# Kernel tuning notes

Measured on AMD Instinct MI355X. Metric: run time of the kernel, lower is better.

The kernel has to match this reference:

```python
import jax, jax.numpy as jnp
import numpy as np

B, D, M, C = 8192, 2048, 8, 1000

def setup_inputs() -> dict:
    key = jax.random.key(0)
    k1, k2, k3, k4, k5 = jax.random.split(key, 5)
    scale = 1.0 / np.sqrt(D)
    return {
        "x": jax.random.normal(k1, (B, D), dtype=jnp.float32),
        "model_weights": jax.random.normal(k2, (M, D, C), dtype=jnp.float32) * scale,
        "model_bias": jax.random.normal(k3, (M, C), dtype=jnp.float32) * 0.01,
        "resnet_weight": jax.random.normal(k4, (D, M * C), dtype=jnp.float32) * scale,
        "resnet_bias": jax.random.normal(k5, (M * C,), dtype=jnp.float32) * 0.01,
    }

def reference(x, model_weights, model_bias, resnet_weight, resnet_bias):
    # Per-submodel logits: [B, M, C]
    outputs = jnp.einsum("bd,mdc->bmc", x, model_weights) + model_bias[None, :, :]
    # Fusion weights from the weighting network: [B, M, C]
    w = (x @ resnet_weight + resnet_bias).reshape(x.shape[0], model_weights.shape[0], model_weights.shape[2])
    # Fused weighted sum over models (replaces the triple Python loop): [B, C]
    result = jnp.sum(outputs * w, axis=1)
    return result
```

## Files before the change

### kernel.cpp

```cpp
#include <hip/hip_runtime.h>
#include <hip/hip_bf16.h>
#include <stdint.h>

#define BDIM 8192
#define DDIM 2048
#define MDIM 8
#define CDIM 1000
#define CPAD 1024
#define NPAD 8192

typedef __attribute__((ext_vector_type(8))) short bf16x8;
typedef __attribute__((ext_vector_type(4))) float f32x4;

__device__ __forceinline__ unsigned short f2bf(float f) {
    union { float f; unsigned u; } v; v.f = f;
    unsigned r = v.u + 0x7fffu + ((v.u >> 16) & 1u);
    return (unsigned short)(r >> 16);
}

__device__ __forceinline__ void gl_lds16(const void* g, void* l) {
    __builtin_amdgcn_global_load_lds(
        (const __attribute__((address_space(1))) void*)g,
        (__attribute__((address_space(3))) void*)l,
        16, 0, 0);
}

__global__ void cast_x_kernel(const float4* __restrict__ x, ushort* __restrict__ xb) {
    int i = blockIdx.x * blockDim.x + threadIdx.x;
    float4 v = x[i];
    ushort4 o;
    o.x = f2bf(v.x); o.y = f2bf(v.y); o.z = f2bf(v.z); o.w = f2bf(v.w);
    *(ushort4*)&xb[(size_t)i * 4] = o;
}

__global__ void prep_w(const float* __restrict__ MW, ushort* __restrict__ wb) {
    __shared__ float tile[32][33];
    int m  = blockIdx.z;
    int c0 = blockIdx.x * 32;
    int d0 = blockIdx.y * 32;
    int tx = threadIdx.x, ty = threadIdx.y;
    const float* src = MW + (size_t)m * DDIM * CDIM;
#pragma unroll
    for (int i = 0; i < 4; i++) {
        int d = d0 + ty + i * 8;
        int c = c0 + tx;
        tile[ty + i * 8][tx] = (c < CDIM) ? src[(size_t)d * CDIM + c] : 0.f;
    }
    __syncthreads();
#pragma unroll
    for (int i = 0; i < 4; i++) {
        int c = c0 + ty + i * 8;
        int d = d0 + tx;
        wb[(size_t)(c * 8 + m) * DDIM + d] = f2bf(tile[tx][ty + i * 8]);
    }
}

__global__ void prep_r(const float* __restrict__ R, ushort* __restrict__ rb) {
    __shared__ float tile[32][33];
    int m  = blockIdx.z;
    int c0 = blockIdx.x * 32;
    int d0 = blockIdx.y * 32;
    int tx = threadIdx.x, ty = threadIdx.y;
#pragma unroll
    for (int i = 0; i < 4; i++) {
        int d = d0 + ty + i * 8;
        int c = c0 + tx;
        tile[ty + i * 8][tx] = (c < CDIM) ? R[(size_t)d * (MDIM * CDIM) + m * CDIM + c] : 0.f;
    }
    __syncthreads();
#pragma unroll
    for (int i = 0; i < 4; i++) {
        int c = c0 + ty + i * 8;
        int d = d0 + tx;
        rb[(size_t)(c * 8 + m) * DDIM + d] = f2bf(tile[tx][ty + i * 8]);
    }
}

__global__ void prep_bias(const float* __restrict__ mb, const float* __restrict__ rbv,
                          float* __restrict__ mb2, float* __restrict__ rb2) {
    int n = blockIdx.x * 256 + threadIdx.x;
    int c = n >> 3, m = n & 7;
    mb2[n] = (c < CDIM) ? mb[m * CDIM + c] : 0.f;
    rb2[n] = (c < CDIM) ? rbv[m * CDIM + c] : 0.f;
}

#define BM 256
#define BN 128
#define BK 64
#define NT (DDIM / BK)

#define STAGE(G, L) do {                                                       \
    _Pragma("unroll")                                                          \
    for (int it_ = 0; it_ < 2; ++it_) {                                        \
        int ci_ = it_ * 512 + tid;                                             \
        int r_ = ci_ >> 3, cc_ = ci_ & 7;                                      \
        gl_lds16((G) + (size_t)r_ * DDIM + (size_t)((cc_ ^ (r_ & 7)) << 3),    \
                 (L) + (size_t)(it_ * 512 + wbase) * 8);                       \
    }                                                                          \
} while (0)

#define LDA(AC, H) do {                                                        \
    _Pragma("unroll")                                                          \
    for (int i_ = 0; i_ < 4; i_++)                                             \
    _Pragma("unroll")                                                          \
    for (int kh_ = 0; kh_ < 2; kh_++) {                                        \
        int row_ = wm * 128 + (H) * 64 + i_ * 16 + (lane & 15);                \
        int cc_ = kh_ * 4 + (lane >> 4);                                       \
        af[i_][kh_] = *(const bf16x8*)&(AC)[row_ * BK + ((cc_ ^ (row_ & 7)) << 3)]; \
    }                                                                          \
} while (0)

#define LDB(BS, BF) do {                                                       \
    _Pragma("unroll")                                                          \
    for (int j_ = 0; j_ < 2; j_++)                                             \
    _Pragma("unroll")                                                          \
    for (int kh_ = 0; kh_ < 2; kh_++) {                                        \
        int row_ = wn * 32 + j_ * 16 + (lane & 15);                            \
        int cc_ = kh_ * 4 + (lane >> 4);                                       \
        BF[j_][kh_] = *(const bf16x8*)&(BS)[row_ * BK + ((cc_ ^ (row_ & 7)) << 3)]; \
    }                                                                          \
} while (0)

#define MM(ACC, H, BF) do {                                                    \
    __builtin_amdgcn_s_setprio(1);                                             \
    _Pragma("unroll")                                                          \
    for (int i_ = 0; i_ < 4; i_++)                                             \
    _Pragma("unroll")                                                          \
    for (int j_ = 0; j_ < 2; j_++)                                             \
    _Pragma("unroll")                                                          \
    for (int kh_ = 0; kh_ < 2; kh_++)                                          \
        ACC[(H) * 4 + i_][j_] = __builtin_amdgcn_mfma_f32_16x16x32_bf16(       \
            af[i_][kh_], BF[j_][kh_], ACC[(H) * 4 + i_][j_], 0, 0, 0);         \
    __builtin_amdgcn_s_setprio(0);                                             \
} while (0)

#define FENCE() asm volatile("" ::: "memory")
#define BARRIER() do { FENCE(); __builtin_amdgcn_s_barrier(); FENCE(); } while (0)

__global__ __launch_bounds__(512, 2) void gemm_fused(
    const ushort* __restrict__ xb, const ushort* __restrict__ wb,
    const ushort* __restrict__ rb,
    const float* __restrict__ mb2, const float* __restrict__ rb2,
    float* __restrict__ out) {
    __shared__ ushort As[2][BM * BK];
    __shared__ ushort B1s[2][BN * BK];
    __shared__ ushort B2s[2][BN * BK];

    int tid   = threadIdx.x;
    int lane  = tid & 63;
    int wid   = tid >> 6;
    int wm    = wid >> 2;
    int wn    = wid & 3;
    int wbase = tid & ~63;

    int wg = blockIdx.x;
    int wgs = (wg & 7) * 256 + (wg >> 3);
    int tile_m = wgs >> 6;
    int tile_n = wgs & 63;
    int brow = tile_m * BM;
    int bn0  = tile_n * BN;

    const ushort* xg  = xb + (size_t)brow * DDIM;
    const ushort* w1g = wb + (size_t)bn0 * DDIM;
    const ushort* w2g = rb + (size_t)bn0 * DDIM;

    f32x4 acc1[8][2] = {};
    f32x4 acc2[8][2] = {};
    bf16x8 af[4][2], bf1[2][2], bf2[2][2];

    STAGE(xg,              As[0]);
    STAGE(xg + 128 * DDIM, As[0] + 128 * BK);
    STAGE(w1g,             B1s[0]);
    STAGE(w2g,             B2s[0]);
    asm volatile("s_waitcnt vmcnt(2)" ::: "memory");
    BARRIER();

#pragma unroll 2
    for (int t = 0; t < NT; ++t) {
        int buf = t & 1;
        ushort* Ac  = As[buf];
        ushort* B1c = B1s[buf];
        ushort* B2c = B2s[buf];
        ushort* An  = As[buf ^ 1];
        ushort* B1n = B1s[buf ^ 1];
        ushort* B2n = B2s[buf ^ 1];
        const int kn = (t + 1) * BK;
        const bool stage = (t + 1 < NT);

        LDA(Ac, 0);
        LDB(B1c, bf1);
        if (stage) STAGE(xg + kn, An);
        BARRIER();
        MM(acc1, 0, bf1);
        if (stage) asm volatile("s_waitcnt vmcnt(2)" ::: "memory");
        else       asm volatile("s_waitcnt vmcnt(0)" ::: "memory");
        BARRIER();

        LDB(B2c, bf2);
        if (stage) STAGE(xg + 128 * DDIM + kn, An + 128 * BK);
        BARRIER();
        MM(acc2, 0, bf2);
        BARRIER();

        LDA(Ac, 1);
        if (stage) STAGE(w1g + kn, B1n);
        BARRIER();
        MM(acc1, 1, bf1);
        BARRIER();

        if (stage) STAGE(w2g + kn, B2n);
        BARRIER();
        MM(acc2, 1, bf2);
        if (stage) asm volatile("s_waitcnt vmcnt(2)" ::: "memory");
        BARRIER();
    }

#pragma unroll
    for (int j = 0; j < 2; j++) {
        int np = bn0 + wn * 32 + j * 16 + (lane & 15);
        float bb1 = mb2[np];
        float bb2 = rb2[np];
        int c = tile_n * 16 + wn * 4 + j * 2 + ((lane >> 3) & 1);
#pragma unroll
        for (int rf = 0; rf < 8; rf++) {
#pragma unroll
            for (int r = 0; r < 4; r++) {
                float p = (acc1[rf][j][r] + bb1) * (acc2[rf][j][r] + bb2);
                p += __shfl_xor(p, 1);
                p += __shfl_xor(p, 2);
                p += __shfl_xor(p, 4);
                if ((lane & 7) == 0 && c < CDIM) {
                    int row = brow + wm * 128 + rf * 16 + ((lane >> 4) << 2) + r;
                    out[(size_t)row * CDIM + c] = p;
                }
            }
        }
    }
}

extern "C" void kernel_launch(void* const* d_in, const int* in_sizes, int n_in,
                              void* d_out, int out_size, void* d_ws, size_t ws_size,
                              hipStream_t stream) {
    const float* x   = (const float*)d_in[0];
    const float* mw  = (const float*)d_in[1];
    const float* mb  = (const float*)d_in[2];
    const float* rw  = (const float*)d_in[3];
    const float* rbv = (const float*)d_in[4];
    float* out = (float*)d_out;

    char* ws = (char*)d_ws;
    ushort* xb  = (ushort*)ws;
    ushort* wb  = (ushort*)(ws + (size_t)33554432);
    ushort* rb  = (ushort*)(ws + (size_t)67108864);
    float*  mb2 = (float*)(ws + (size_t)100663296);
    float*  rb2 = (float*)(ws + (size_t)100696064);

    cast_x_kernel<<<BDIM * DDIM / (256 * 4), 256, 0, stream>>>((const float4*)x, xb);
    prep_w<<<dim3(CPAD / 32, DDIM / 32, MDIM), dim3(32, 8), 0, stream>>>(mw, wb);
    prep_r<<<dim3(CPAD / 32, DDIM / 32, MDIM), dim3(32, 8), 0, stream>>>(rw, rb);
    prep_bias<<<NPAD / 256, 256, 0, stream>>>(mb, rbv, mb2, rb2);

    gemm_fused<<<dim3((BDIM / BM) * (NPAD / BN)), 512, 0, stream>>>(xb, wb, rb, mb2, rb2, out);
}
```

Measured before the change: 605.6 us.

## Reorder A-row ownership and reschedule global-to-LDS staging with a peeled last iteration

Each wave's A rows now come half from the first 128-row half of the tile and half from the second, rather than a contiguous 128-row block, and the output row mapping is changed to match. The prefetch order is rearranged so the second A half is staged last, the B tiles are staged earlier, and the vmcnt waits are placed to fit that order. The final K iteration is peeled out so the steady-state loop has no stage conditionals, and its last two MFMA groups run back to back. The aim is to overlap global loads with compute more evenly and drop branching, at the cost of more waitcnt points that must be correct for the data to be ready.

Result: faster. 578.2 us (-4.5%).

```diff
diff --git a/kernel.cpp b/kernel.cpp
--- a/kernel.cpp
+++ b/kernel.cpp
@@ -104,7 +104,7 @@
     for (int i_ = 0; i_ < 4; i_++)                                             \
     _Pragma("unroll")                                                          \
     for (int kh_ = 0; kh_ < 2; kh_++) {                                        \
-        int row_ = wm * 128 + (H) * 64 + i_ * 16 + (lane & 15);                \
+        int row_ = (H) * 128 + wm * 64 + i_ * 16 + (lane & 15);                \
         int cc_ = kh_ * 4 + (lane >> 4);                                       \
         af[i_][kh_] = *(const bf16x8*)&(AC)[row_ * BK + ((cc_ ^ (row_ & 7)) << 3)]; \
     }                                                                          \
@@ -136,6 +136,7 @@
 
 #define FENCE() asm volatile("" ::: "memory")
 #define BARRIER() do { FENCE(); __builtin_amdgcn_s_barrier(); FENCE(); } while (0)
+#define WAITV(N) asm volatile("s_waitcnt vmcnt(" #N ")" ::: "memory")
 
 __global__ __launch_bounds__(512, 2) void gemm_fused(
     const ushort* __restrict__ xb, const ushort* __restrict__ wb,
@@ -169,14 +170,14 @@
     bf16x8 af[4][2], bf1[2][2], bf2[2][2];
 
     STAGE(xg,              As[0]);
-    STAGE(xg + 128 * DDIM, As[0] + 128 * BK);
     STAGE(w1g,             B1s[0]);
     STAGE(w2g,             B2s[0]);
-    asm volatile("s_waitcnt vmcnt(2)" ::: "memory");
+    STAGE(xg + 128 * DDIM, As[0] + 128 * BK);
+    WAITV(4);
     BARRIER();
 
 #pragma unroll 2
-    for (int t = 0; t < NT; ++t) {
+    for (int t = 0; t < NT - 1; ++t) {
         int buf = t & 1;
         ushort* Ac  = As[buf];
         ushort* B1c = B1s[buf];
@@ -185,34 +186,57 @@
         ushort* B1n = B1s[buf ^ 1];
         ushort* B2n = B2s[buf ^ 1];
         const int kn = (t + 1) * BK;
-        const bool stage = (t + 1 < NT);
 
         LDA(Ac, 0);
         LDB(B1c, bf1);
-        if (stage) STAGE(xg + kn, An);
+        STAGE(xg + kn, An);
         BARRIER();
         MM(acc1, 0, bf1);
-        if (stage) asm volatile("s_waitcnt vmcnt(2)" ::: "memory");
-        else       asm volatile("s_waitcnt vmcnt(0)" ::: "memory");
+        WAITV(4);
         BARRIER();
 
         LDB(B2c, bf2);
-        if (stage) STAGE(xg + 128 * DDIM + kn, An + 128 * BK);
+        STAGE(w1g + kn, B1n);
         BARRIER();
         MM(acc2, 0, bf2);
+        WAITV(4);
         BARRIER();
 
         LDA(Ac, 1);
-        if (stage) STAGE(w1g + kn, B1n);
+        STAGE(w2g + kn, B2n);
         BARRIER();
         MM(acc1, 1, bf1);
         BARRIER();
 
-        if (stage) STAGE(w2g + kn, B2n);
+        STAGE(xg + 128 * DDIM + kn, An + 128 * BK);
         BARRIER();
         MM(acc2, 1, bf2);
-        if (stage) asm volatile("s_waitcnt vmcnt(2)" ::: "memory");
-        BARRIER();
+        WAITV(4);
+        BARRIER();
+    }
+
+    {
+        ushort* Ac  = As[(NT - 1) & 1];
+        ushort* B1c = B1s[(NT - 1) & 1];
+        ushort* B2c = B2s[(NT - 1) & 1];
+
+        LDA(Ac, 0);
+        LDB(B1c, bf1);
+        BARRIER();
+        MM(acc1, 0, bf1);
+        WAITV(2);
+        BARRIER();
+
+        LDB(B2c, bf2);
+        BARRIER();
+        MM(acc2, 0, bf2);
+        WAITV(0);
+        BARRIER();
+
+        LDA(Ac, 1);
+        BARRIER();
+        MM(acc1, 1, bf1);
+        MM(acc2, 1, bf2);
     }
 
 #pragma unroll
@@ -230,7 +254,8 @@
                 p += __shfl_xor(p, 2);
                 p += __shfl_xor(p, 4);
                 if ((lane & 7) == 0 && c < CDIM) {
-                    int row = brow + wm * 128 + rf * 16 + ((lane >> 4) << 2) + r;
+                    int row = brow + (rf >> 2) * 128 + wm * 64 + (rf & 3) * 16
+                              + ((lane >> 4) << 2) + r;
                     out[(size_t)row * CDIM + c] = p;
                 }
             }
```
